# Performance work log

Hardware: AMD Instinct MI355X
Metric: run time of the kernel (lower is better)

Reference implementation:

```python
import jax, jax.numpy as jnp
import numpy as np

INPUT_DIM, OUTPUT_DIM = 128, 256
FPS_FACTOR, KNN = 14, 10


def fps(pcd, K):
    """Farthest point sampling. pcd: [B,N,3] -> (points [B,K,3], indices [B,K]).
    Deterministic start at index 0 (pytorch3d uses first/random point)."""
    B, N, _ = pcd.shape
    first = jnp.zeros((B,), jnp.int32)
    init_d = jnp.full((B, N), 1e10, pcd.dtype)

    def step(carry, _):
        dists, last = carry
        lp = jnp.take_along_axis(pcd, last[:, None, None], axis=1)  # [B,1,3]
        d = jnp.sum((pcd - lp) ** 2, axis=-1)                        # [B,N]
        dists = jnp.minimum(dists, d)
        nxt = jnp.argmax(dists, axis=-1).astype(jnp.int32)
        return (dists, nxt), nxt

    (_, _), rest = jax.lax.scan(step, (init_d, first), None, length=K - 1)
    idx = jnp.concatenate([first[None, :], rest], axis=0).T  # [B,K]
    pts = jnp.take_along_axis(pcd, idx[..., None], axis=1)   # [B,K,3]
    return pts, idx


def knn_idx(q, p, k):
    """q:[B,Q,3], p:[B,N,3] -> nearest-neighbor indices [B,Q,k] (squared L2)."""
    d = (jnp.sum(q * q, -1)[:, :, None] + jnp.sum(p * p, -1)[:, None, :]
         - 2.0 * jnp.einsum('bqc,bnc->bqn', q, p))
    _, idx = jax.lax.top_k(-d, k)
    return idx


_bgather = jax.vmap(lambda a, i: a[i])  # per-batch fancy gather


def setup_inputs() -> dict:
    key = jax.random.key(0)
    k1, k2, k3, k4, k5 = jax.random.split(key, 5)
    B, N = 4, 16384
    tgt = jax.random.normal(k1, (B, N, INPUT_DIM), jnp.float32)
    pcd_x = jax.random.normal(k2, (B, N, 3), jnp.float32)
    pcd_v = jax.random.normal(k3, (B, N, 3, 3), jnp.float32)
    W = jax.random.normal(k4, (INPUT_DIM, OUTPUT_DIM), jnp.float32) / np.sqrt(INPUT_DIM)
    b = jax.random.normal(k5, (OUTPUT_DIM,), jnp.float32) * 0.01
    return {"tgt": tgt, "pcd_x": pcd_x, "pcd_v": pcd_v, "W": W, "b": b}


def reference(tgt, pcd_x, pcd_v, W, b):
    B, N, D = tgt.shape
    n_out = N // FPS_FACTOR
    out_pcd_x, out_indices = fps(pcd_x, n_out)          # [B,n_out,3], [B,n_out]
    nn = knn_idx(out_pcd_x, pcd_x, KNN)                 # [B,n_out,k]

    knn_pcd = _bgather(pcd_x, nn)                       # [B,n_out,k,3]
    query_f = jnp.take_along_axis(tgt, out_indices[..., None], axis=1)  # [B,n_out,D]
    query_c = out_pcd_x
    query_v = _bgather(pcd_v, out_indices)              # [B,n_out,V,3]
    key_f = _bgather(tgt, nn)                           # [B,n_out,k,D]
    key_c = knn_pcd
    key_v = _bgather(pcd_v, nn)                         # [B,n_out,k,V,3]

    # flatten (B*n_out) super-point groups, project features
    _query_f = query_f.reshape(-1, D)[:, None, :] @ W + b          # [B*n_out,1,O]
    _key_f = key_f.reshape(-1, KNN, D) @ W + b                     # [B*n_out,k,O]
    del _key_f, key_c, key_v  # consumed by the (identity stand-in) transformer

    # NOTE: URSATransformer stand-in = identity on the projected query features
    out_query_f = _query_f.reshape(B, n_out, OUTPUT_DIM)
    return out_query_f, query_c, query_v
```

## Files before the change

### kernel.cpp

```cpp
#include <hip/hip_runtime.h>

constexpr int B_   = 4;
constexpr int N_   = 16384;
constexpr int NOUT = 1170;
constexpr int D_   = 128;
constexpr int O_   = 256;

typedef float f32x2 __attribute__((ext_vector_type(2)));
typedef unsigned long long u64;

template <int CTRL>
__device__ __forceinline__ float dpp_fmax(float x) {
  int yi = __builtin_amdgcn_update_dpp(__float_as_int(x), __float_as_int(x),
                                       CTRL, 0xF, 0xF, false);
  return fmaxf(x, __int_as_float(yi));
}
template <int CTRL>
__device__ __forceinline__ int dpp_imin(int x) {
  int y = __builtin_amdgcn_update_dpp(x, x, CTRL, 0xF, 0xF, false);
  return y < x ? y : x;
}

constexpr int TPB_FPS = 1024;
constexpr int PPT   = 16;
constexpr int NPR   = 8;
constexpr int NW    = TPB_FPS / 64;
constexpr size_t LDS_BYTES = (size_t)2 * N_ * 4 + NW * 8 + 16;

__global__ __launch_bounds__(TPB_FPS, 1)
void fps_kernel(const float* __restrict__ pcd_x,
                int* __restrict__ sel,
                float* __restrict__ out_c) {
  extern __shared__ float smem[];
  float*  xs     = smem;
  float*  ys     = smem + N_;
  float2* s_pair = (float2*)(smem + 2 * N_);
  float*  s_z    = (float*)(s_pair + NW);

  const int b = blockIdx.x, t = threadIdx.x;
  const int lane = t & 63, w = t >> 6;
  const float* __restrict__ P = pcd_x + (size_t)b * N_ * 3;

  f32x2 zs[NPR], dm[NPR];
#pragma unroll
  for (int j = 0; j < NPR; ++j) {
    const int p0 = 2 * t + j * 2048;
    const float x0 = P[p0 * 3 + 0], y0 = P[p0 * 3 + 1], z0 = P[p0 * 3 + 2];
    const float x1 = P[p0 * 3 + 3], y1 = P[p0 * 3 + 4], z1 = P[p0 * 3 + 5];
    *reinterpret_cast<f32x2*>(&xs[p0]) = f32x2{x0, x1};
    *reinterpret_cast<f32x2*>(&ys[p0]) = f32x2{y0, y1};
    zs[j] = f32x2{z0, z1};
    dm[j] = f32x2{1e10f, 1e10f};
  }
  __syncthreads();

  float lx = P[0], ly = P[1], lz = P[2];
  if (t == 0) {
    sel[b * NOUT + 0] = 0;
    out_c[((size_t)b * NOUT + 0) * 3 + 0] = lx;
    out_c[((size_t)b * NOUT + 0) * 3 + 1] = ly;
    out_c[((size_t)b * NOUT + 0) * 3 + 2] = lz;
  }

  for (int step = 1; step < NOUT; ++step) {
    const float nx = __int_as_float(__float_as_int(lx) ^ 0x80000000);
    const float ny = __int_as_float(__float_as_int(ly) ^ 0x80000000);
    const float nz = __int_as_float(__float_as_int(lz) ^ 0x80000000);
    const f32x2 nlx = {nx, nx}, nly = {ny, ny}, nlz = {nz, nz};

    f32x2 bvv = {-1.0f, -1.0f};
    {
#pragma clang fp contract(off)
#pragma unroll
      for (int j = 0; j < NPR; ++j) {
        const int p0 = 2 * t + j * 2048;
        const f32x2 xv = *reinterpret_cast<const f32x2*>(&xs[p0]);
        const f32x2 yv = *reinterpret_cast<const f32x2*>(&ys[p0]);
        const f32x2 dx = xv + nlx;
        const f32x2 dy = yv + nly;
        const f32x2 dz = zs[j] + nlz;
        const f32x2 s  = (dx * dx + dy * dy) + dz * dz;
        dm[j] = __builtin_elementwise_min(dm[j], s);
        bvv   = __builtin_elementwise_max(bvv, dm[j]);
      }
    }
    const float bv = fmaxf(bvv.x, bvv.y);

    asm volatile("" : "+v"(zs[0]), "+v"(zs[1]), "+v"(zs[2]), "+v"(zs[3]),
                      "+v"(zs[4]), "+v"(zs[5]), "+v"(zs[6]), "+v"(zs[7]));
    asm volatile("" : "+v"(dm[0]), "+v"(dm[1]), "+v"(dm[2]), "+v"(dm[3]),
                      "+v"(dm[4]), "+v"(dm[5]), "+v"(dm[6]), "+v"(dm[7]));

    float wm = bv;
    wm = dpp_fmax<0xB1>(wm);
    wm = dpp_fmax<0x4E>(wm);
    wm = dpp_fmax<0x141>(wm);
    wm = dpp_fmax<0x140>(wm);
    wm = dpp_fmax<0x142>(wm);
    wm = dpp_fmax<0x143>(wm);
    const float wmax =
        __int_as_float(__builtin_amdgcn_readlane(__float_as_int(wm), 63));

    int bi = 0x7fffffff;
#pragma unroll
    for (int j = NPR - 1; j >= 0; --j) {
      if (dm[j].y == bv) bi = 2 * t + j * 2048 + 1;
      if (dm[j].x == bv) bi = 2 * t + j * 2048;
    }
    int mi = (bv == wmax) ? bi : 0x7fffffff;
    mi = dpp_imin<0xB1>(mi);
    mi = dpp_imin<0x4E>(mi);
    mi = dpp_imin<0x141>(mi);
    mi = dpp_imin<0x140>(mi);
    mi = dpp_imin<0x142>(mi);
    mi = dpp_imin<0x143>(mi);
    const int widx = __builtin_amdgcn_readlane(mi, 63);

    if (lane == 0) s_pair[w] = make_float2(wmax, __int_as_float(widx));
    __syncthreads();

    const float2 e = s_pair[lane & (NW - 1)];
    float gv = e.x;
    gv = dpp_fmax<0xB1>(gv);
    gv = dpp_fmax<0x4E>(gv);
    gv = dpp_fmax<0x141>(gv);
    gv = dpp_fmax<0x140>(gv);
    int m2 = (e.x == gv) ? __float_as_int(e.y) : 0x7fffffff;
    m2 = dpp_imin<0xB1>(m2);
    m2 = dpp_imin<0x4E>(m2);
    m2 = dpp_imin<0x141>(m2);
    m2 = dpp_imin<0x140>(m2);
    const int ri = __builtin_amdgcn_readfirstlane(m2);

    if (t == ((ri & 2047) >> 1)) {
      const int oj = ri >> 11, oh = ri & 1;
      s_z[0] = oh ? zs[oj].y : zs[oj].x;
    }
    __syncthreads();

    lx = xs[ri];
    ly = ys[ri];
    lz = s_z[0];
    if (t == 0) {
      sel[b * NOUT + step] = ri;
      out_c[((size_t)b * NOUT + step) * 3 + 0] = lx;
      out_c[((size_t)b * NOUT + step) * 3 + 1] = ly;
      out_c[((size_t)b * NOUT + step) * 3 + 2] = lz;
    }
  }
}

constexpr int TPB_PROJ = 256;
constexpr int RPB = 4;

__global__ __launch_bounds__(TPB_PROJ)
void proj_kernel(const float* __restrict__ tgt,
                 const float* __restrict__ pcd_v,
                 const float* __restrict__ W,
                 const float* __restrict__ bias,
                 const int* __restrict__ sel,
                 float* __restrict__ out_f,
                 float* __restrict__ out_v) {
  const int t = threadIdx.x;
  const int row0 = blockIdx.x * RPB;
  __shared__ float sA[RPB * D_];
  __shared__ int   sIdx[RPB];
  if (t < RPB) {
    const int row = row0 + t;
    const int b = row / NOUT;
    sIdx[t] = b * N_ + sel[row];
  }
  __syncthreads();
#pragma unroll
  for (int l = 0; l < RPB * D_ / TPB_PROJ; ++l) {
    const int e = t + l * TPB_PROJ;
    const int r = e >> 7, k = e & (D_ - 1);
    sA[e] = tgt[(size_t)sIdx[r] * D_ + k];
  }
  __syncthreads();
  float acc0 = 0.f, acc1 = 0.f, acc2 = 0.f, acc3 = 0.f;
#pragma unroll 8
  for (int k = 0; k < D_; ++k) {
    const float w = W[k * O_ + t];
    acc0 = fmaf(sA[0 * D_ + k], w, acc0);
    acc1 = fmaf(sA[1 * D_ + k], w, acc1);
    acc2 = fmaf(sA[2 * D_ + k], w, acc2);
    acc3 = fmaf(sA[3 * D_ + k], w, acc3);
  }
  const float bb = bias[t];
  out_f[(size_t)(row0 + 0) * O_ + t] = acc0 + bb;
  out_f[(size_t)(row0 + 1) * O_ + t] = acc1 + bb;
  out_f[(size_t)(row0 + 2) * O_ + t] = acc2 + bb;
  out_f[(size_t)(row0 + 3) * O_ + t] = acc3 + bb;
  if (t < RPB * 9) {
    const int r = t / 9, e = t - r * 9;
    out_v[(size_t)(row0 + r) * 9 + e] = pcd_v[(size_t)sIdx[r] * 9 + e];
  }
}

extern "C" void kernel_launch(void* const* d_in, const int* in_sizes, int n_in,
                              void* d_out, int out_size, void* d_ws, size_t ws_size,
                              hipStream_t stream) {
  const float* tgt   = (const float*)d_in[0];
  const float* pcd_x = (const float*)d_in[1];
  const float* pcd_v = (const float*)d_in[2];
  const float* W     = (const float*)d_in[3];
  const float* bias  = (const float*)d_in[4];

  float* out   = (float*)d_out;
  float* out_f = out;
  float* out_c = out + (size_t)B_ * NOUT * O_;
  float* out_v = out_c + (size_t)B_ * NOUT * 3;

  int* sel = (int*)d_ws;

  hipLaunchKernelGGL(fps_kernel, dim3(B_), dim3(TPB_FPS), LDS_BYTES, stream,
                     pcd_x, sel, out_c);
  hipLaunchKernelGGL(proj_kernel, dim3(B_ * NOUT / RPB), dim3(TPB_PROJ), 0, stream,
                     tgt, pcd_v, W, bias, sel, out_f, out_v);
}
```

Before: 2.126 ms.

## Make FPS point ownership contiguous and resolve argmax index via ballot

Each thread now owns a contiguous run of 16 points, with x/y stored in LDS as interleaved f32x2 slots. Because ownership is contiguous, the lowest index among tied maxima can be found by picking the first matching warp and then the first matching lane, both via ballot. This drops the per-warp and cross-warp DPP integer-min reductions and the separate z broadcast. The winning lane writes coordinates and index to LDS and global memory directly, cutting reduction depth on the serial FPS critical path.

```diff
diff --git a/kernel.cpp b/kernel.cpp
--- a/kernel.cpp
+++ b/kernel.cpp
@@ -15,27 +15,21 @@
                                        CTRL, 0xF, 0xF, false);
   return fmaxf(x, __int_as_float(yi));
 }
-template <int CTRL>
-__device__ __forceinline__ int dpp_imin(int x) {
-  int y = __builtin_amdgcn_update_dpp(x, x, CTRL, 0xF, 0xF, false);
-  return y < x ? y : x;
-}
 
 constexpr int TPB_FPS = 1024;
-constexpr int PPT   = 16;
 constexpr int NPR   = 8;
 constexpr int NW    = TPB_FPS / 64;
-constexpr size_t LDS_BYTES = (size_t)2 * N_ * 4 + NW * 8 + 16;
+constexpr size_t LDS_BYTES = (size_t)2 * N_ * 4 + NW * 4 + 16;
 
 __global__ __launch_bounds__(TPB_FPS, 1)
 void fps_kernel(const float* __restrict__ pcd_x,
                 int* __restrict__ sel,
                 float* __restrict__ out_c) {
-  extern __shared__ float smem[];
-  float*  xs     = smem;
-  float*  ys     = smem + N_;
-  float2* s_pair = (float2*)(smem + 2 * N_);
-  float*  s_z    = (float*)(s_pair + NW);
+  extern __shared__ char smem_raw[];
+  f32x2*  xs2   = (f32x2*)smem_raw;
+  f32x2*  ys2   = xs2 + 8 * 1024;
+  float*  s_val = (float*)(ys2 + 8 * 1024);
+  float4* s_res = (float4*)(s_val + NW);
 
   const int b = blockIdx.x, t = threadIdx.x;
   const int lane = t & 63, w = t >> 6;
@@ -43,14 +37,12 @@
 
   f32x2 zs[NPR], dm[NPR];
 #pragma unroll
-  for (int j = 0; j < NPR; ++j) {
-    const int p0 = 2 * t + j * 2048;
-    const float x0 = P[p0 * 3 + 0], y0 = P[p0 * 3 + 1], z0 = P[p0 * 3 + 2];
-    const float x1 = P[p0 * 3 + 3], y1 = P[p0 * 3 + 4], z1 = P[p0 * 3 + 5];
-    *reinterpret_cast<f32x2*>(&xs[p0]) = f32x2{x0, x1};
-    *reinterpret_cast<f32x2*>(&ys[p0]) = f32x2{y0, y1};
-    zs[j] = f32x2{z0, z1};
-    dm[j] = f32x2{1e10f, 1e10f};
+  for (int h = 0; h < NPR; ++h) {
+    const int p0 = 16 * t + 2 * h;
+    xs2[h * 1024 + t] = f32x2{P[p0 * 3 + 0], P[p0 * 3 + 3]};
+    ys2[h * 1024 + t] = f32x2{P[p0 * 3 + 1], P[p0 * 3 + 4]};
+    zs[h] = f32x2{P[p0 * 3 + 2], P[p0 * 3 + 5]};
+    dm[h] = f32x2{1e10f, 1e10f};
   }
   __syncthreads();
 
@@ -72,16 +64,15 @@
     {
 #pragma clang fp contract(off)
 #pragma unroll
-      for (int j = 0; j < NPR; ++j) {
-        const int p0 = 2 * t + j * 2048;
-        const f32x2 xv = *reinterpret_cast<const f32x2*>(&xs[p0]);
-        const f32x2 yv = *reinterpret_cast<const f32x2*>(&ys[p0]);
+      for (int h = 0; h < NPR; ++h) {
+        const f32x2 xv = xs2[h * 1024 + t];
+        const f32x2 yv = ys2[h * 1024 + t];
         const f32x2 dx = xv + nlx;
         const f32x2 dy = yv + nly;
-        const f32x2 dz = zs[j] + nlz;
+        const f32x2 dz = zs[h] + nlz;
         const f32x2 s  = (dx * dx + dy * dy) + dz * dz;
-        dm[j] = __builtin_elementwise_min(dm[j], s);
-        bvv   = __builtin_elementwise_max(bvv, dm[j]);
+        dm[h] = __builtin_elementwise_min(dm[h], s);
+        bvv   = __builtin_elementwise_max(bvv, dm[h]);
       }
     }
     const float bv = fmaxf(bvv.x, bvv.y);
@@ -100,53 +91,45 @@
     wm = dpp_fmax<0x143>(wm);
     const float wmax =
         __int_as_float(__builtin_amdgcn_readlane(__float_as_int(wm), 63));
-
-    int bi = 0x7fffffff;
-#pragma unroll
-    for (int j = NPR - 1; j >= 0; --j) {
-      if (dm[j].y == bv) bi = 2 * t + j * 2048 + 1;
-      if (dm[j].x == bv) bi = 2 * t + j * 2048;
-    }
-    int mi = (bv == wmax) ? bi : 0x7fffffff;
-    mi = dpp_imin<0xB1>(mi);
-    mi = dpp_imin<0x4E>(mi);
-    mi = dpp_imin<0x141>(mi);
-    mi = dpp_imin<0x140>(mi);
-    mi = dpp_imin<0x142>(mi);
-    mi = dpp_imin<0x143>(mi);
-    const int widx = __builtin_amdgcn_readlane(mi, 63);
-
-    if (lane == 0) s_pair[w] = make_float2(wmax, __int_as_float(widx));
+    if (lane == 0) s_val[w] = wmax;
     __syncthreads();
 
-    const float2 e = s_pair[lane & (NW - 1)];
-    float gv = e.x;
+    const float e = s_val[lane & (NW - 1)];
+    float gv = e;
     gv = dpp_fmax<0xB1>(gv);
     gv = dpp_fmax<0x4E>(gv);
     gv = dpp_fmax<0x141>(gv);
     gv = dpp_fmax<0x140>(gv);
-    int m2 = (e.x == gv) ? __float_as_int(e.y) : 0x7fffffff;
-    m2 = dpp_imin<0xB1>(m2);
-    m2 = dpp_imin<0x4E>(m2);
-    m2 = dpp_imin<0x141>(m2);
-    m2 = dpp_imin<0x140>(m2);
-    const int ri = __builtin_amdgcn_readfirstlane(m2);
-
-    if (t == ((ri & 2047) >> 1)) {
-      const int oj = ri >> 11, oh = ri & 1;
-      s_z[0] = oh ? zs[oj].y : zs[oj].x;
+
+    const u64 wwm = __ballot((lane < NW) && (e == gv));
+    const int ww = __builtin_ctzll(wwm);
+
+    if (w == ww && bv == gv) {
+      const u64 am = __ballot(true);
+      if (lane == __builtin_ctzll(am)) {
+        int bi = 0;
+#pragma unroll
+        for (int h = NPR - 1; h >= 0; --h) {
+          if (dm[h].y == bv) bi = 16 * t + 2 * h + 1;
+          if (dm[h].x == bv) bi = 16 * t + 2 * h;
+        }
+        const int loc = bi & 15, hh = loc >> 1, hf = loc & 1;
+        const f32x2 xv = xs2[hh * 1024 + t];
+        const f32x2 yv = ys2[hh * 1024 + t];
+        const float wx = hf ? xv.y : xv.x;
+        const float wy = hf ? yv.y : yv.x;
+        const float wz = hf ? zs[hh].y : zs[hh].x;
+        s_res[0] = make_float4(wx, wy, wz, __int_as_float(bi));
+        sel[b * NOUT + step] = bi;
+        out_c[((size_t)b * NOUT + step) * 3 + 0] = wx;
+        out_c[((size_t)b * NOUT + step) * 3 + 1] = wy;
+        out_c[((size_t)b * NOUT + step) * 3 + 2] = wz;
+      }
     }
     __syncthreads();
 
-    lx = xs[ri];
-    ly = ys[ri];
-    lz = s_z[0];
-    if (t == 0) {
-      sel[b * NOUT + step] = ri;
-      out_c[((size_t)b * NOUT + step) * 3 + 0] = lx;
-      out_c[((size_t)b * NOUT + step) * 3 + 1] = ly;
-      out_c[((size_t)b * NOUT + step) * 3 + 2] = lz;
-    }
+    const float4 r = s_res[0];
+    lx = r.x; ly = r.y; lz = r.z;
   }
 }
 
```

New measurement: 1.975 ms. 1.08x faster.
